# Kernel optimization log

Hardware: AMD Instinct MI355X
Metric: run time of the kernel (lower is better)

Reference implementation:

```python
import jax, jax.numpy as jnp
import numpy as np

IN_C = 32
OUT_C = 32
N_POLY = 3   # radial polynomial order
L_POLY = 3   # theta polynomial order
M_POLY = 3   # phi polynomial order
CONV_NUMS = 16
EPS = 1e-8


def _knn_select(pos, space_points_num, outpoint_num, conv_num):
    """Strided center sampling + KNN within each space. pos: [P,3].
    Returns global neighbor indices [space_num*outpoint_num, conv_num]."""
    P = pos.shape[0]
    S = P // space_points_num
    pos3 = pos.reshape(S, space_points_num, 3)
    stride = space_points_num // outpoint_num
    c_idx = jnp.arange(outpoint_num) * stride                       # [O]
    cpos = pos3[:, c_idx]                                           # [S,O,3]
    d2 = jnp.sum((cpos[:, :, None, :] - pos3[:, None, :, :]) ** 2, -1)  # [S,O,Ps]
    _, idx = jax.lax.top_k(-d2, conv_num)                           # [S,O,conv]
    idx = idx + (jnp.arange(S) * space_points_num)[:, None, None]
    return idx.reshape(S * outpoint_num, conv_num)


def _dcconv_forward(position_matrix, channel_matrix, coeff, bias, neighbor_indices, conv_num):
    K = neighbor_indices.shape[0]
    # --- CoordinateTransformer: gather, center, PCA rotate, spherical ---
    nbr = position_matrix[neighbor_indices]            # [K,conv,3]
    centers = nbr.mean(axis=1)                         # [K,3]
    local = nbr - centers[:, None, :]                  # [K,conv,3]
    cov = jnp.einsum('kci,kcj->kij', local, local) / conv_num
    _, V = jnp.linalg.eigh(cov)                        # [K,3,3] principal axes
    local_pca = jnp.einsum('kci,kij->kcj', local, V)   # rotate into PCA frame
    x, y, z = local_pca[..., 0], local_pca[..., 1], local_pca[..., 2]
    r = jnp.sqrt(x * x + y * y + z * z + EPS)          # [K,conv]
    theta = jnp.arccos(jnp.clip(z / r, -1.0, 1.0))
    phi = jnp.arctan2(y, x)
    # --- local features: [C_in, K, conv] (matches permute(2,0,1)) ---
    feat = channel_matrix[neighbor_indices].transpose(2, 0, 1)
    # --- DCConv3dKernelPolynomials: separable polynomial basis ---
    rp = r[..., None] ** jnp.arange(N_POLY, dtype=r.dtype)          # [K,conv,N]
    tp = theta[..., None] ** jnp.arange(L_POLY, dtype=r.dtype)      # [K,conv,L]
    pp = phi[..., None] ** jnp.arange(M_POLY, dtype=r.dtype)        # [K,conv,M]
    basis = jnp.einsum('kcn,kcl,kcm->kcnlm', rp, tp, pp)            # [K,conv,N,L,M]
    kernel_weights = jnp.einsum('kcnlm,oinlm->oikc', basis, coeff)  # [O,I,K,conv]
    # --- AggregationLayer: weighted sum over in-channels and neighbors ---
    out = jnp.einsum('ikc,oikc->ok', feat, kernel_weights)          # [O,K]
    output = out.T + bias                                           # [K,O]
    # --- resnet branch: all-ones kernel -> per-point feature sum ---
    resnet_output = jnp.broadcast_to(feat.sum(axis=(0, 2))[:, None], (K, OUT_C))
    return centers, output, resnet_output


def setup_inputs() -> dict:
    key = jax.random.key(0)
    k1, k2, k3 = jax.random.split(key, 3)
    P = 16384
    return {
        "position_matrix": jax.random.normal(k1, (P, 3), jnp.float32),
        "channel_matrix": jax.random.normal(k2, (P, IN_C), jnp.float32),
        "space_points_num": 1024,
        "outpoint_num": 256,
        "coeff": jax.random.normal(k3, (OUT_C, IN_C, N_POLY, L_POLY, M_POLY), jnp.float32) * 0.1,
        "bias": jnp.zeros((OUT_C,), jnp.float32),
    }


def reference(position_matrix, channel_matrix, space_points_num, outpoint_num, coeff, bias):
    conv_num = min(space_points_num - outpoint_num + 1, CONV_NUMS)
    neighbor_indices = _knn_select(position_matrix, space_points_num, outpoint_num, conv_num)
    return _dcconv_forward(position_matrix, channel_matrix, coeff, bias, neighbor_indices, conv_num)
```

## Files before the change

### kernel.cpp

```cpp
#include <hip/hip_runtime.h>
#include <math.h>

#define NSPACE 16
#define SPN    1024
#define OPN    256
#define STRIDE 4
#define CONV   16
#define KTOT   4096
#define INC    32
#define OUTC   32
#define NB     27
#define EPS_R  1e-8f

#define OFF_OUT 12288
#define OFF_RES 143360

typedef float v2f __attribute__((ext_vector_type(2)));

#define UPDPP __builtin_amdgcn_update_dpp

__device__ __forceinline__ float wave_min64_bcast(float m) {
  int t;
  t = UPDPP(__float_as_int(m), __float_as_int(m), 0x111, 0xf, 0xf, false);
  m = fminf(m, __int_as_float(t));
  t = UPDPP(__float_as_int(m), __float_as_int(m), 0x112, 0xf, 0xf, false);
  m = fminf(m, __int_as_float(t));
  t = UPDPP(__float_as_int(m), __float_as_int(m), 0x114, 0xf, 0xf, false);
  m = fminf(m, __int_as_float(t));
  t = UPDPP(__float_as_int(m), __float_as_int(m), 0x118, 0xf, 0xf, false);
  m = fminf(m, __int_as_float(t));
  t = UPDPP(__float_as_int(m), __float_as_int(m), 0x142, 0xa, 0xf, false);
  m = fminf(m, __int_as_float(t));
  t = UPDPP(__float_as_int(m), __float_as_int(m), 0x143, 0xc, 0xf, false);
  m = fminf(m, __int_as_float(t));
  return __int_as_float(__builtin_amdgcn_readlane(__float_as_int(m), 63));
}

__device__ __forceinline__ float wave_sum64_bcast(float m) {
  int t;
  t = UPDPP(0, __float_as_int(m), 0x111, 0xf, 0xf, true); m += __int_as_float(t);
  t = UPDPP(0, __float_as_int(m), 0x112, 0xf, 0xf, true); m += __int_as_float(t);
  t = UPDPP(0, __float_as_int(m), 0x114, 0xf, 0xf, true); m += __int_as_float(t);
  t = UPDPP(0, __float_as_int(m), 0x118, 0xf, 0xf, true); m += __int_as_float(t);
  t = UPDPP(0, __float_as_int(m), 0x142, 0xa, 0xf, true); m += __int_as_float(t);
  t = UPDPP(0, __float_as_int(m), 0x143, 0xc, 0xf, true); m += __int_as_float(t);
  return __int_as_float(__builtin_amdgcn_readlane(__float_as_int(m), 63));
}

__device__ __forceinline__ float group32_sum(float m) {
  int t;
  t = UPDPP(0, __float_as_int(m), 0x111, 0xf, 0xf, true); m += __int_as_float(t);
  t = UPDPP(0, __float_as_int(m), 0x112, 0xf, 0xf, true); m += __int_as_float(t);
  t = UPDPP(0, __float_as_int(m), 0x114, 0xf, 0xf, true); m += __int_as_float(t);
  t = UPDPP(0, __float_as_int(m), 0x118, 0xf, 0xf, true); m += __int_as_float(t);
  t = UPDPP(0, __float_as_int(m), 0x142, 0xa, 0xf, true); m += __int_as_float(t);
  return m;
}


#define EIGH_Z_PARAMS                                                         \
  float &z00, float &z01, float &z02, float &z10, float &z11, float &z12,     \
  float &z20, float &z21, float &z22
#define EIGH_Z_ARGS z00, z01, z02, z10, z11, z12, z20, z21, z22

#define ROT01(c, s)                                              \
  { float _t;                                                    \
    _t = z01; z01 = (c) * _t - (s) * z00; z00 = (s) * _t + (c) * z00; \
    _t = z11; z11 = (c) * _t - (s) * z10; z10 = (s) * _t + (c) * z10; \
    _t = z21; z21 = (c) * _t - (s) * z20; z20 = (s) * _t + (c) * z20; }
#define ROT12(c, s)                                              \
  { float _t;                                                    \
    _t = z02; z02 = (c) * _t - (s) * z01; z01 = (s) * _t + (c) * z01; \
    _t = z12; z12 = (c) * _t - (s) * z11; z11 = (s) * _t + (c) * z11; \
    _t = z22; z22 = (c) * _t - (s) * z21; z21 = (s) * _t + (c) * z21; }
#define SWAP01 { float _t; _t = z00; z00 = z01; z01 = _t; _t = z10; z10 = z11; z11 = _t; _t = z20; z20 = z21; z21 = _t; }
#define SWAP02 { float _t; _t = z00; z00 = z02; z02 = _t; _t = z10; z10 = z12; z12 = _t; _t = z20; z20 = z22; z22 = _t; }
#define SWAP12 { float _t; _t = z01; z01 = z02; z02 = _t; _t = z11; z11 = z12; z12 = _t; _t = z21; z21 = z22; z22 = _t; }

__device__ __forceinline__ float f_sign(float a, float b) {
  return (b >= 0.0f) ? fabsf(a) : -fabsf(a);
}

__device__ __forceinline__ float slapy2(float x, float y) {
  float xa = fabsf(x), ya = fabsf(y);
  float w = fmaxf(xa, ya), zz = fminf(xa, ya);
  if (zz == 0.0f) return w;
  float q = zz / w;
  return w * __fsqrt_rn(1.0f + q * q);
}

__device__ __forceinline__ void slartg_(float f, float g, float* c, float* s, float* r) {
  const float safmin = 1.1754943508e-38f;
  const float safmax = 8.5070591730e+37f;
  const float rtmin  = 1.0842021725e-19f;
  const float rtmax  = 9.2233720369e+18f;
  float f1 = fabsf(f), g1 = fabsf(g);
  if (g == 0.0f) {
    *c = 1.0f; *s = 0.0f; *r = f;
  } else if (f == 0.0f) {
    *c = 0.0f; *s = (g >= 0.0f) ? 1.0f : -1.0f; *r = g1;
  } else if (f1 > rtmin && f1 < rtmax && g1 > rtmin && g1 < rtmax) {
    float d = __fsqrt_rn(f * f + g * g);
    *c = f1 / d;
    *r = (f >= 0.0f) ? d : -d;
    *s = g / (*r);
  } else {
    float u = fminf(safmax, fmaxf(safmin, fmaxf(f1, g1)));
    float fs = f / u, gs = g / u;
    float d = __fsqrt_rn(fs * fs + gs * gs);
    *c = fabsf(fs) / d;
    float rr = (f >= 0.0f) ? d : -d;
    *s = gs / rr;
    *r = rr * u;
  }
}

__device__ __forceinline__ void slaev2_(float a, float b, float c,
                                        float* rt1, float* rt2, float* cs1, float* sn1) {
  float sm = a + c;
  float df = a - c;
  float adf = fabsf(df);
  float tb = b + b;
  float ab = fabsf(tb);
  float acmx, acmn;
  if (fabsf(a) > fabsf(c)) { acmx = a; acmn = c; } else { acmx = c; acmn = a; }
  float rt;
  if (adf > ab)      { float q = ab / adf; rt = adf * __fsqrt_rn(1.0f + q * q); }
  else if (adf < ab) { float q = adf / ab; rt = ab  * __fsqrt_rn(1.0f + q * q); }
  else               { rt = ab * __fsqrt_rn(2.0f); }
  int sgn1;
  if (sm < 0.0f) {
    *rt1 = 0.5f * (sm - rt); sgn1 = -1;
    *rt2 = (acmx / *rt1) * acmn - (b / *rt1) * b;
  } else if (sm > 0.0f) {
    *rt1 = 0.5f * (sm + rt); sgn1 = 1;
    *rt2 = (acmx / *rt1) * acmn - (b / *rt1) * b;
  } else {
    *rt1 = 0.5f * rt; *rt2 = -0.5f * rt; sgn1 = 1;
  }
  float cs; int sgn2;
  if (df >= 0.0f) { cs = df + rt; sgn2 = 1; } else { cs = df - rt; sgn2 = -1; }
  float acs = fabsf(cs);
  if (acs > ab) {
    float ct = -tb / cs;
    *sn1 = 1.0f / __fsqrt_rn(1.0f + ct * ct);
    *cs1 = ct * (*sn1);
  } else {
    if (ab == 0.0f) { *cs1 = 1.0f; *sn1 = 0.0f; }
    else {
      float tn = -cs / tb;
      *cs1 = 1.0f / __fsqrt_rn(1.0f + tn * tn);
      *sn1 = tn * (*cs1);
    }
  }
  if (sgn1 == sgn2) { float tn = *cs1; *cs1 = -(*sn1); *sn1 = tn; }
}

__device__ __forceinline__ void steqr2_01(float& dA, float& eA, float& dB,
                                          bool ql, EIGH_Z_PARAMS) {
  const float eps2 = 3.5527136788e-15f, safmin = 1.1754943508e-38f;
  float tst = eA * eA;
  float thr = ql ? (eps2 * fabsf(dA)) * fabsf(dB) + safmin
                 : (eps2 * fabsf(dB)) * fabsf(dA) + safmin;
  if (tst <= thr) { eA = 0.0f; return; }
  float rt1, rt2, c, s;
  slaev2_(dA, eA, dB, &rt1, &rt2, &c, &s);
  ROT01(c, s);
  dA = rt1; dB = rt2; eA = 0.0f;
}

__device__ __forceinline__ void steqr2_12(float& dA, float& eA, float& dB,
                                          bool ql, EIGH_Z_PARAMS) {
  const float eps2 = 3.5527136788e-15f, safmin = 1.1754943508e-38f;
  float tst = eA * eA;
  float thr = ql ? (eps2 * fabsf(dA)) * fabsf(dB) + safmin
                 : (eps2 * fabsf(dB)) * fabsf(dA) + safmin;
  if (tst <= thr) { eA = 0.0f; return; }
  float rt1, rt2, c, s;
  slaev2_(dA, eA, dB, &rt1, &rt2, &c, &s);
  ROT12(c, s);
  dA = rt1; dB = rt2; eA = 0.0f;
}

__device__ __forceinline__ void steqr_ql3(float& d1, float& d2, float& d3,
                                          float& e1, float& e2, int& jtot,
                                          EIGH_Z_PARAMS) {
  const float eps2 = 3.5527136788e-15f, safmin = 1.1754943508e-38f;
  int l = 1;
  while (true) {
    if (l == 1) {
      if (e1 * e1 <= (eps2 * fabsf(d1)) * fabsf(d2) + safmin) { e1 = 0.0f; l = 2; continue; }
      if (e2 * e2 <= (eps2 * fabsf(d2)) * fabsf(d3) + safmin) {
        e2 = 0.0f;
        float rt1, rt2, c, s;
        slaev2_(d1, e1, d2, &rt1, &rt2, &c, &s);
        ROT01(c, s);
        d1 = rt1; d2 = rt2; e1 = 0.0f;
        l = 3; continue;
      }
      if (jtot == 90) return;
      jtot++;
      float p = d1;
      float g = (d2 - p) / (2.0f * e1);
      float r = slapy2(g, 1.0f);
      g = d3 - p + (e1 / (g + f_sign(r, g)));
      float s = 1.0f, c = 1.0f; p = 0.0f;
      float f, b, wc1, wc2, ws1, ws2;
      f = s * e2; b = c * e2;
      slartg_(g, f, &c, &s, &r);
      g = d3 - p;
      r = (d2 - g) * s + 2.0f * c * b;
      p = s * r;
      d3 = g + p;
      g = c * r - b;
      wc2 = c; ws2 = -s;
      f = s * e1; b = c * e1;
      slartg_(g, f, &c, &s, &r);
      e2 = r;
      g = d2 - p;
      r = (d1 - g) * s + 2.0f * c * b;
      p = s * r;
      d2 = g + p;
      g = c * r - b;
      wc1 = c; ws1 = -s;
      if (wc2 != 1.0f || ws2 != 0.0f) ROT12(wc2, ws2);
      if (wc1 != 1.0f || ws1 != 0.0f) ROT01(wc1, ws1);
      d1 = d1 - p;
      e1 = g;
      continue;
    }
    if (l == 2) {
      if (e2 * e2 <= (eps2 * fabsf(d2)) * fabsf(d3) + safmin) { e2 = 0.0f; l = 3; continue; }
      float rt1, rt2, c, s;
      slaev2_(d2, e2, d3, &rt1, &rt2, &c, &s);
      ROT12(c, s);
      d2 = rt1; d3 = rt2; e2 = 0.0f;
      return;
    }
    return;
  }
}

__device__ __forceinline__ void steqr_qr3(float& d1, float& d2, float& d3,
                                          float& e1, float& e2, int& jtot,
                                          EIGH_Z_PARAMS) {
  const float eps2 = 3.5527136788e-15f, safmin = 1.1754943508e-38f;
  int l = 3;
  while (true) {
    if (l == 3) {
      if (e2 * e2 <= (eps2 * fabsf(d3)) * fabsf(d2) + safmin) { e2 = 0.0f; l = 2; continue; }
      if (e1 * e1 <= (eps2 * fabsf(d2)) * fabsf(d1) + safmin) {
        e1 = 0.0f;
        float rt1, rt2, c, s;
        slaev2_(d2, e2, d3, &rt1, &rt2, &c, &s);
        ROT12(c, s);
        d2 = rt1; d3 = rt2; e2 = 0.0f;
        l = 1; continue;
      }
      if (jtot == 90) return;
      jtot++;
      float p = d3;
      float g = (d2 - p) / (2.0f * e2);
      float r = slapy2(g, 1.0f);
      g = d1 - p + (e2 / (g + f_sign(r, g)));
      float s = 1.0f, c = 1.0f; p = 0.0f;
      float f, b, wc1, wc2, ws1, ws2;
      f = s * e1; b = c * e1;
      slartg_(g, f, &c, &s, &r);
      g = d1 - p;
      r = (d2 - g) * s + 2.0f * c * b;
      p = s * r;
      d1 = g + p;
      g = c * r - b;
      wc1 = c; ws1 = s;
      f = s * e2; b = c * e2;
      slartg_(g, f, &c, &s, &r);
      e1 = r;
      g = d2 - p;
      r = (d3 - g) * s + 2.0f * c * b;
      p = s * r;
      d2 = g + p;
      g = c * r - b;
      wc2 = c; ws2 = s;
      if (wc1 != 1.0f || ws1 != 0.0f) ROT01(wc1, ws1);
      if (wc2 != 1.0f || ws2 != 0.0f) ROT12(wc2, ws2);
      d3 = d3 - p;
      e2 = g;
      continue;
    }
    if (l == 2) {
      if (e1 * e1 <= (eps2 * fabsf(d2)) * fabsf(d1) + safmin) { e1 = 0.0f; l = 1; continue; }
      float rt1, rt2, c, s;
      slaev2_(d1, e1, d2, &rt1, &rt2, &c, &s);
      ROT01(c, s);
      d1 = rt1; d2 = rt2; e1 = 0.0f;
      return;
    }
    return;
  }
}

__device__ __forceinline__ void ssteqr3s(float& d1, float& d2, float& d3,
                                         float& e1, float& e2, EIGH_Z_PARAMS) {
  const float eps    = 5.9604644775e-08f;
  const float ssfmax = 3.0744573457e+18f;
  const float ssfmin = 3.0517578125e-05f;
  int jtot = 0;
  int m;
  {
    float tst = fabsf(e1);
    if (tst == 0.0f) m = 1;
    else if (tst <= (__fsqrt_rn(fabsf(d1)) * __fsqrt_rn(fabsf(d2))) * eps) { e1 = 0.0f; m = 1; }
    else {
      tst = fabsf(e2);
      if (tst == 0.0f) m = 2;
      else if (tst <= (__fsqrt_rn(fabsf(d2)) * __fsqrt_rn(fabsf(d3))) * eps) { e2 = 0.0f; m = 2; }
      else m = 3;
    }
  }
  if (m == 3) {
    float anorm = fmaxf(fmaxf(fabsf(d1), fabsf(d2)), fabsf(d3));
    anorm = fmaxf(anorm, fmaxf(fabsf(e1), fabsf(e2)));
    if (anorm != 0.0f) {
      int iscale = 0; float mul;
      if (anorm > ssfmax) {
        iscale = 1; mul = ssfmax / anorm;
        d1 *= mul; d2 *= mul; d3 *= mul; e1 *= mul; e2 *= mul;
      } else if (anorm < ssfmin) {
        iscale = 2; mul = ssfmin / anorm;
        d1 *= mul; d2 *= mul; d3 *= mul; e1 *= mul; e2 *= mul;
      }
      if (fabsf(d3) < fabsf(d1)) steqr_qr3(d1, d2, d3, e1, e2, jtot, EIGH_Z_ARGS);
      else                       steqr_ql3(d1, d2, d3, e1, e2, jtot, EIGH_Z_ARGS);
      if (iscale == 1) {
        mul = anorm / ssfmax;
        d1 *= mul; d2 *= mul; d3 *= mul; e1 *= mul; e2 *= mul;
      } else if (iscale == 2) {
        mul = anorm / ssfmin;
        d1 *= mul; d2 *= mul; d3 *= mul; e1 *= mul; e2 *= mul;
      }
    }
  } else if (m == 2) {
    float anorm = fmaxf(fmaxf(fabsf(d1), fabsf(d2)), fabsf(e1));
    if (anorm != 0.0f) {
      int iscale = 0; float mul;
      if (anorm > ssfmax) { iscale = 1; mul = ssfmax / anorm; d1 *= mul; d2 *= mul; e1 *= mul; }
      else if (anorm < ssfmin) { iscale = 2; mul = ssfmin / anorm; d1 *= mul; d2 *= mul; e1 *= mul; }
      steqr2_01(d1, e1, d2, !(fabsf(d2) < fabsf(d1)), EIGH_Z_ARGS);
      if (iscale == 1) { mul = anorm / ssfmax; d1 *= mul; d2 *= mul; e1 *= mul; }
      else if (iscale == 2) { mul = anorm / ssfmin; d1 *= mul; d2 *= mul; e1 *= mul; }
    }
  } else {
    int m2;
    float tst = fabsf(e2);
    if (tst == 0.0f) m2 = 2;
    else if (tst <= (__fsqrt_rn(fabsf(d2)) * __fsqrt_rn(fabsf(d3))) * eps) { e2 = 0.0f; m2 = 2; }
    else m2 = 3;
    if (m2 == 3) {
      float anorm = fmaxf(fmaxf(fabsf(d2), fabsf(d3)), fabsf(e2));
      if (anorm != 0.0f) {
        int iscale = 0; float mul;
        if (anorm > ssfmax) { iscale = 1; mul = ssfmax / anorm; d2 *= mul; d3 *= mul; e2 *= mul; }
        else if (anorm < ssfmin) { iscale = 2; mul = ssfmin / anorm; d2 *= mul; d3 *= mul; e2 *= mul; }
        steqr2_12(d2, e2, d3, !(fabsf(d3) < fabsf(d2)), EIGH_Z_ARGS);
        if (iscale == 1) { mul = anorm / ssfmax; d2 *= mul; d3 *= mul; e2 *= mul; }
        else if (iscale == 2) { mul = anorm / ssfmin; d2 *= mul; d3 *= mul; e2 *= mul; }
      }
    }
  }
  {
    int k = 1; float p = d1;
    if (d2 < p) { k = 2; p = d2; }
    if (d3 < p) { k = 3; p = d3; }
    if (k == 2)      { d2 = d1; d1 = p; SWAP01; }
    else if (k == 3) { d3 = d1; d1 = p; SWAP02; }
    if (d3 < d2) { p = d3; d3 = d2; d2 = p; SWAP12; }
  }
}

__device__ __forceinline__ void eigh3(float a11, float a21, float a31,
                                      float a22, float a32, float a33,
                                      EIGH_Z_PARAMS) {
  float tau1 = 0.0f, v3 = 0.0f, e1;
  float xnorm = fabsf(a31);
  if (xnorm == 0.0f) {
    tau1 = 0.0f;
    e1 = a21;
    v3 = 0.0f;
  } else {
    float beta = -f_sign(slapy2(a21, xnorm), a21);
    tau1 = (beta - a21) / beta;
    v3 = a31 / (a21 - beta);
    e1 = beta;
  }
  if (tau1 != 0.0f) {
    float x1 = tau1 * (a22 + a32 * v3);
    float x2 = tau1 * (a32 + a33 * v3);
    float alpha = -0.5f * tau1 * (x1 + x2 * v3);
    float w1 = x1 + alpha;
    float w2 = x2 + alpha * v3;
    a22 = a22 - w1 - w1;
    a32 = a32 - v3 * w1 - w2;
    a33 = a33 - v3 * w2 - w2 * v3;
  }
  float d1 = a11, d2 = a22, d3 = a33, e2 = a32;
  z00 = 1.0f; z01 = 0.0f; z02 = 0.0f;
  z10 = 0.0f; z11 = 1.0f; z12 = 0.0f;
  z20 = 0.0f; z21 = 0.0f; z22 = 1.0f;
  ssteqr3s(d1, d2, d3, e1, e2, EIGH_Z_ARGS);
  if (tau1 != 0.0f) {
    float tt;
    tt = z10 + v3 * z20; z10 -= tau1 * tt; z20 -= tau1 * tt * v3;
    tt = z11 + v3 * z21; z11 -= tau1 * tt; z21 -= tau1 * tt * v3;
    tt = z12 + v3 * z22; z12 -= tau1 * tt; z22 -= tau1 * tt * v3;
  }
}


#define CE(i, j)                                                  \
  {                                                               \
    unsigned long long ta = K[i], tb = K[j];                      \
    bool sw = tb < ta;                                            \
    K[i] = sw ? tb : ta;                                          \
    K[j] = sw ? ta : tb;                                          \
  }

#define RFL(x) __int_as_float(__builtin_amdgcn_readfirstlane(__float_as_int(x)))

__global__ __launch_bounds__(256, 4) void dcconv_fused(
    const float* __restrict__ pos, const float* __restrict__ chan,
    const float* __restrict__ coeff, const float* __restrict__ bias,
    float* __restrict__ out) {
  const int t    = threadIdx.x;
  const int wv   = t >> 6;
  const int lane = t & 63;
  const int kglob = blockIdx.x * 4 + wv;
  const int sp   = kglob >> 8;
  const int ci   = kglob & 255;
  const int base = sp * SPN;

  __shared__ __align__(16) float basis_sh[4][CONV][28];
  __shared__ __align__(16) float feat_sh[4][CONV][INC];
  __shared__ __align__(16) float G_sh[4][INC][28];

  const int cgl = base + ci * STRIDE;
  const float cx = pos[cgl * 3 + 0];
  const float cy = pos[cgl * 3 + 1];
  const float cz = pos[cgl * 3 + 2];

  unsigned long long K[16];
#pragma unroll
  for (int u = 0; u < 16; ++u) {
    const int j = u * 64 + lane;
    const float px = pos[(base + j) * 3 + 0];
    const float py = pos[(base + j) * 3 + 1];
    const float pz = pos[(base + j) * 3 + 2];
    float dx = __fsub_rn(cx, px), dy = __fsub_rn(cy, py), dz = __fsub_rn(cz, pz);
    float d2 = __fadd_rn(__fadd_rn(__fmul_rn(dx, dx), __fmul_rn(dy, dy)),
                         __fmul_rn(dz, dz));
    K[u] = (((unsigned long long)__float_as_uint(d2)) << 32) | (unsigned)j;
  }

  CE(0, 1) CE(2, 3) CE(4, 5) CE(6, 7) CE(8, 9) CE(10, 11) CE(12, 13) CE(14, 15)
  CE(0, 2) CE(1, 3) CE(4, 6) CE(5, 7) CE(8, 10) CE(9, 11) CE(12, 14) CE(13, 15)
  CE(1, 2) CE(5, 6) CE(9, 10) CE(13, 14)
  CE(0, 4) CE(1, 5) CE(2, 6) CE(3, 7) CE(8, 12) CE(9, 13) CE(10, 14) CE(11, 15)
  CE(2, 4) CE(3, 5) CE(10, 12) CE(11, 13)
  CE(1, 2) CE(3, 4) CE(5, 6) CE(9, 10) CE(11, 12) CE(13, 14)
  CE(0, 8) CE(1, 9) CE(2, 10) CE(3, 11) CE(4, 12) CE(5, 13) CE(6, 14) CE(7, 15)
  CE(4, 8) CE(5, 9) CE(6, 10) CE(7, 11)
  CE(2, 4) CE(3, 5) CE(6, 8) CE(7, 9) CE(10, 12) CE(11, 13)
  CE(1, 2) CE(3, 4) CE(5, 6) CE(7, 8) CE(9, 10) CE(11, 12) CE(13, 14)

  int myidx = cgl;
#pragma unroll 1
  for (int it = 0; it < CONV; ++it) {
    const float f0 = __uint_as_float((unsigned)(K[0] >> 32));
    const float m = wave_min64_bcast(f0);
    const unsigned long long msk = __ballot(f0 == m);
    const int wl = (int)__builtin_ctzll(msk);
    const int widx = __builtin_amdgcn_readlane((int)(unsigned)(K[0] & 0xffffffffu), wl);
    if (lane == it) myidx = base + widx;
    const bool on = (lane == wl);
#pragma unroll
    for (int u = 0; u < 15; ++u) K[u] = on ? K[u + 1] : K[u];
    K[15] = on ? ~0ull : K[15];
  }

  float nx = 0.0f, ny = 0.0f, nz = 0.0f;
  if (lane < CONV) {
    const float* pp = pos + myidx * 3;
    nx = pp[0]; ny = pp[1]; nz = pp[2];
  }

  const int hc = lane >> 5;
  const int ifeat = lane & 31;
  float fv0, fv1, fv2, fv3, fv4, fv5, fv6, fv7;
  {
    int g;
    g = __shfl(myidx,  0 + hc); fv0 = chan[g * INC + ifeat];
    g = __shfl(myidx,  2 + hc); fv1 = chan[g * INC + ifeat];
    g = __shfl(myidx,  4 + hc); fv2 = chan[g * INC + ifeat];
    g = __shfl(myidx,  6 + hc); fv3 = chan[g * INC + ifeat];
    g = __shfl(myidx,  8 + hc); fv4 = chan[g * INC + ifeat];
    g = __shfl(myidx, 10 + hc); fv5 = chan[g * INC + ifeat];
    g = __shfl(myidx, 12 + hc); fv6 = chan[g * INC + ifeat];
    g = __shfl(myidx, 14 + hc); fv7 = chan[g * INC + ifeat];
  }

  const float mx = wave_sum64_bcast(nx) * 0.0625f;
  const float my = wave_sum64_bcast(ny) * 0.0625f;
  const float mz = wave_sum64_bcast(nz) * 0.0625f;
  if (lane == 0) {
    out[kglob * 3 + 0] = mx; out[kglob * 3 + 1] = my; out[kglob * 3 + 2] = mz;
  }
  const float lx = nx - mx, ly = ny - my, lz = nz - mz;
  const float lxm = (lane < CONV) ? lx : 0.0f;
  const float lym = (lane < CONV) ? ly : 0.0f;
  const float lzm = (lane < CONV) ? lz : 0.0f;
  const float inv = 1.0f / (float)CONV;
  const float c00 = wave_sum64_bcast(lxm * lxm) * inv;
  const float c10 = wave_sum64_bcast(lym * lxm) * inv;
  const float c20 = wave_sum64_bcast(lzm * lxm) * inv;
  const float c11 = wave_sum64_bcast(lym * lym) * inv;
  const float c21 = wave_sum64_bcast(lzm * lym) * inv;
  const float c22 = wave_sum64_bcast(lzm * lzm) * inv;

  float V00 = 0, V01 = 0, V02 = 0, V10 = 0, V11 = 0, V12 = 0,
        V20 = 0, V21 = 0, V22 = 0;
  if (lane == 0) {
    eigh3(c00, c10, c20, c11, c21, c22,
          V00, V01, V02, V10, V11, V12, V20, V21, V22);
  }
  V00 = RFL(V00); V01 = RFL(V01); V02 = RFL(V02);
  V10 = RFL(V10); V11 = RFL(V11); V12 = RFL(V12);
  V20 = RFL(V20); V21 = RFL(V21); V22 = RFL(V22);

  if (lane < CONV) {
    float x = lx * V00 + ly * V10 + lz * V20;
    float y = lx * V01 + ly * V11 + lz * V21;
    float z = lx * V02 + ly * V12 + lz * V22;
    float r = __fsqrt_rn(x * x + y * y + z * z + EPS_R);
    float ct = fminf(fmaxf(z / r, -1.0f), 1.0f);
    float theta = acosf(ct);
    float phi = atan2f(y, x);
    const float r1 = r, r2 = r * r;
    const float t1 = theta, t2 = theta * theta;
    const float p1 = phi, p2 = phi * phi;
    float4* bp = (float4*)(&basis_sh[wv][lane][0]);
    bp[0] = make_float4(1.0f,      p1,        p2,        t1);
    bp[1] = make_float4(t1 * p1,   t1 * p2,   t2,        t2 * p1);
    bp[2] = make_float4(t2 * p2,   r1,        r1 * p1,   r1 * p2);
    bp[3] = make_float4(r1 * t1,   r1 * t1 * p1, r1 * t1 * p2, r1 * t2);
    bp[4] = make_float4(r1 * t2 * p1, r1 * t2 * p2, r2,  r2 * p1);
    bp[5] = make_float4(r2 * p2,   r2 * t1,   r2 * t1 * p1, r2 * t1 * p2);
    bp[6] = make_float4(r2 * t2,   r2 * t2 * p1, r2 * t2 * p2, 0.0f);
  }

  feat_sh[wv][ 0 + hc][ifeat] = fv0;
  feat_sh[wv][ 2 + hc][ifeat] = fv1;
  feat_sh[wv][ 4 + hc][ifeat] = fv2;
  feat_sh[wv][ 6 + hc][ifeat] = fv3;
  feat_sh[wv][ 8 + hc][ifeat] = fv4;
  feat_sh[wv][10 + hc][ifeat] = fv5;
  feat_sh[wv][12 + hc][ifeat] = fv6;
  feat_sh[wv][14 + hc][ifeat] = fv7;
  float s_loc = ((fv0 + fv1) + (fv2 + fv3)) + ((fv4 + fv5) + (fv6 + fv7));
  const float sres = wave_sum64_bcast(s_loc);
  if (lane < OUTC) out[OFF_RES + kglob * OUTC + lane] = sres;

  {
    const int gi = lane >> 1;
    const int jh = lane & 1;
    const int jr0 = jh ? 12 : 0;
    v2f a2[8];
#pragma unroll
    for (int q = 0; q < 8; ++q) a2[q] = (v2f)(0.0f);
#pragma unroll
    for (int c = 0; c < CONV; ++c) {
      const float f = feat_sh[wv][c][gi];
      const v2f f2 = (v2f)(f);
      const float4* bp = (const float4*)(&basis_sh[wv][c][jr0]);
#pragma unroll
      for (int q = 0; q < 4; ++q) {
        const float4 v4 = bp[q];
        v2f blo; blo.x = v4.x; blo.y = v4.y;
        v2f bhi; bhi.x = v4.z; bhi.y = v4.w;
        a2[2 * q + 0] += f2 * blo;
        a2[2 * q + 1] += f2 * bhi;
      }
    }
    if (jh == 0) {
      float4* gp = (float4*)(&G_sh[wv][gi][0]);
      gp[0] = make_float4(a2[0].x, a2[0].y, a2[1].x, a2[1].y);
      gp[1] = make_float4(a2[2].x, a2[2].y, a2[3].x, a2[3].y);
      gp[2] = make_float4(a2[4].x, a2[4].y, a2[5].x, a2[5].y);
      gp[3] = make_float4(a2[6].x, a2[6].y, a2[7].x, a2[7].y);
    } else {
      float4* gp = (float4*)(&G_sh[wv][gi][16]);
      gp[0] = make_float4(a2[2].x, a2[2].y, a2[3].x, a2[3].y);
      gp[1] = make_float4(a2[4].x, a2[4].y, a2[5].x, a2[5].y);
      gp[2] = make_float4(a2[6].x, a2[6].y, a2[7].x, a2[7].y);
    }
  }

  __syncthreads();

  {
    const int ir = t & 31;
    const int oh = t >> 5;
    const int l32 = lane & 31;
#pragma unroll
    for (int p = 0; p < 2; ++p) {
      const int o0 = oh * 4 + p * 2;
      const float* cA = coeff + (o0 * INC + ir) * NB;
      const float* cB = coeff + ((o0 + 1) * INC + ir) * NB;
      v2f c0p[14], c1p[14];
#pragma unroll
      for (int q = 0; q < 13; ++q) {
        c0p[q].x = cA[2 * q]; c0p[q].y = cA[2 * q + 1];
        c1p[q].x = cB[2 * q]; c1p[q].y = cB[2 * q + 1];
      }
      c0p[13].x = cA[26]; c0p[13].y = 0.0f;
      c1p[13].x = cB[26]; c1p[13].y = 0.0f;
      float s0c0 = 0, s0c1 = 0, s0c2 = 0, s0c3 = 0;
      float s1c0 = 0, s1c1 = 0, s1c2 = 0, s1c3 = 0;
#pragma unroll
      for (int cc = 0; cc < 4; ++cc) {
        const float4* gp = (const float4*)(&G_sh[cc][ir][0]);
        v2f a0 = (v2f)(0.0f), a1 = (v2f)(0.0f);
#pragma unroll
        for (int q = 0; q < 7; ++q) {
          const float4 v4 = gp[q];
          v2f glo; glo.x = v4.x; glo.y = v4.y;
          v2f ghi; ghi.x = v4.z; ghi.y = v4.w;
          a0 += glo * c0p[2 * q + 0];
          a0 += ghi * c0p[2 * q + 1];
          a1 += glo * c1p[2 * q + 0];
          a1 += ghi * c1p[2 * q + 1];
        }
        const float s0 = a0.x + a0.y;
        const float s1 = a1.x + a1.y;
        if (cc == 0) { s0c0 = s0; s1c0 = s1; }
        else if (cc == 1) { s0c1 = s0; s1c1 = s1; }
        else if (cc == 2) { s0c2 = s0; s1c2 = s1; }
        else { s0c3 = s0; s1c3 = s1; }
      }
      s0c0 = group32_sum(s0c0); s0c1 = group32_sum(s0c1);
      s0c2 = group32_sum(s0c2); s0c3 = group32_sum(s0c3);
      s1c0 = group32_sum(s1c0); s1c1 = group32_sum(s1c1);
      s1c2 = group32_sum(s1c2); s1c3 = group32_sum(s1c3);
      if (l32 == 31) {
        const float b0 = bias[o0], b1 = bias[o0 + 1];
        const int kb = blockIdx.x * 4;
        out[OFF_OUT + (kb + 0) * OUTC + o0] = s0c0 + b0;
        out[OFF_OUT + (kb + 1) * OUTC + o0] = s0c1 + b0;
        out[OFF_OUT + (kb + 2) * OUTC + o0] = s0c2 + b0;
        out[OFF_OUT + (kb + 3) * OUTC + o0] = s0c3 + b0;
        out[OFF_OUT + (kb + 0) * OUTC + o0 + 1] = s1c0 + b1;
        out[OFF_OUT + (kb + 1) * OUTC + o0 + 1] = s1c1 + b1;
        out[OFF_OUT + (kb + 2) * OUTC + o0 + 1] = s1c2 + b1;
        out[OFF_OUT + (kb + 3) * OUTC + o0 + 1] = s1c3 + b1;
      }
    }
  }
}

extern "C" void kernel_launch(void* const* d_in, const int* in_sizes, int n_in,
                              void* d_out, int out_size, void* d_ws, size_t ws_size,
                              hipStream_t stream) {
  const float* pos   = (const float*)d_in[0];
  const float* chan  = (const float*)d_in[1];
  const float* coeff = (const float*)d_in[4];
  const float* bias  = (const float*)d_in[5];
  float* out = (float*)d_out;
  dcconv_fused<<<dim3(KTOT / 4), dim3(256), 0, stream>>>(pos, chan, coeff, bias, out);
}
```

Baseline: 34.26 us.

## Flatten G to contiguous IN*NB layout and contract coeff rows with float4 loads

The per-channel G matrix is stored densely as a flat [INC*27] array per wave instead of padded rows of 28. The final contraction is remapped so each group of 8 threads owns one output channel and streams that channel's 864 coefficients as coalesced float4 loads. This replaces strided scalar coefficient loads and 32-lane reductions with a reduction over 8 lanes. In exchange, G is now written with scalar LDS stores and the float4 LDS reads of G may hit more bank conflicts.

```diff
diff --git a/kernel.cpp b/kernel.cpp
--- a/kernel.cpp
+++ b/kernel.cpp
@@ -47,13 +47,11 @@
   return __int_as_float(__builtin_amdgcn_readlane(__float_as_int(m), 63));
 }
 
-__device__ __forceinline__ float group32_sum(float m) {
+__device__ __forceinline__ float group8_sum(float m) {
   int t;
   t = UPDPP(0, __float_as_int(m), 0x111, 0xf, 0xf, true); m += __int_as_float(t);
   t = UPDPP(0, __float_as_int(m), 0x112, 0xf, 0xf, true); m += __int_as_float(t);
   t = UPDPP(0, __float_as_int(m), 0x114, 0xf, 0xf, true); m += __int_as_float(t);
-  t = UPDPP(0, __float_as_int(m), 0x118, 0xf, 0xf, true); m += __int_as_float(t);
-  t = UPDPP(0, __float_as_int(m), 0x142, 0xa, 0xf, true); m += __int_as_float(t);
   return m;
 }
 
@@ -441,7 +439,7 @@
 
   __shared__ __align__(16) float basis_sh[4][CONV][28];
   __shared__ __align__(16) float feat_sh[4][CONV][INC];
-  __shared__ __align__(16) float G_sh[4][INC][28];
+  __shared__ __align__(16) float G4_sh[4][INC * NB];
 
   const int cgl = base + ci * STRIDE;
   const float cx = pos[cgl * 3 + 0];
@@ -590,78 +588,64 @@
         a2[2 * q + 1] += f2 * bhi;
       }
     }
+    float* gq = &G4_sh[wv][gi * NB];
     if (jh == 0) {
-      float4* gp = (float4*)(&G_sh[wv][gi][0]);
-      gp[0] = make_float4(a2[0].x, a2[0].y, a2[1].x, a2[1].y);
-      gp[1] = make_float4(a2[2].x, a2[2].y, a2[3].x, a2[3].y);
-      gp[2] = make_float4(a2[4].x, a2[4].y, a2[5].x, a2[5].y);
-      gp[3] = make_float4(a2[6].x, a2[6].y, a2[7].x, a2[7].y);
+#pragma unroll
+      for (int jj = 0; jj < 14; ++jj)
+        gq[jj] = (jj & 1) ? a2[jj >> 1].y : a2[jj >> 1].x;
     } else {
-      float4* gp = (float4*)(&G_sh[wv][gi][16]);
-      gp[0] = make_float4(a2[2].x, a2[2].y, a2[3].x, a2[3].y);
-      gp[1] = make_float4(a2[4].x, a2[4].y, a2[5].x, a2[5].y);
-      gp[2] = make_float4(a2[6].x, a2[6].y, a2[7].x, a2[7].y);
+#pragma unroll
+      for (int jj = 14; jj < 27; ++jj) {
+        const int m = jj - 12;
+        gq[jj] = (m & 1) ? a2[m >> 1].y : a2[m >> 1].x;
+      }
     }
   }
 
   __syncthreads();
 
   {
-    const int ir = t & 31;
-    const int oh = t >> 5;
-    const int l32 = lane & 31;
-#pragma unroll
-    for (int p = 0; p < 2; ++p) {
-      const int o0 = oh * 4 + p * 2;
-      const float* cA = coeff + (o0 * INC + ir) * NB;
-      const float* cB = coeff + ((o0 + 1) * INC + ir) * NB;
-      v2f c0p[14], c1p[14];
-#pragma unroll
-      for (int q = 0; q < 13; ++q) {
-        c0p[q].x = cA[2 * q]; c0p[q].y = cA[2 * q + 1];
-        c1p[q].x = cB[2 * q]; c1p[q].y = cB[2 * q + 1];
-      }
-      c0p[13].x = cA[26]; c0p[13].y = 0.0f;
-      c1p[13].x = cB[26]; c1p[13].y = 0.0f;
-      float s0c0 = 0, s0c1 = 0, s0c2 = 0, s0c3 = 0;
-      float s1c0 = 0, s1c1 = 0, s1c2 = 0, s1c3 = 0;
-#pragma unroll
-      for (int cc = 0; cc < 4; ++cc) {
-        const float4* gp = (const float4*)(&G_sh[cc][ir][0]);
-        v2f a0 = (v2f)(0.0f), a1 = (v2f)(0.0f);
-#pragma unroll
-        for (int q = 0; q < 7; ++q) {
-          const float4 v4 = gp[q];
-          v2f glo; glo.x = v4.x; glo.y = v4.y;
-          v2f ghi; ghi.x = v4.z; ghi.y = v4.w;
-          a0 += glo * c0p[2 * q + 0];
-          a0 += ghi * c0p[2 * q + 1];
-          a1 += glo * c1p[2 * q + 0];
-          a1 += ghi * c1p[2 * q + 1];
-        }
-        const float s0 = a0.x + a0.y;
-        const float s1 = a1.x + a1.y;
-        if (cc == 0) { s0c0 = s0; s1c0 = s1; }
-        else if (cc == 1) { s0c1 = s0; s1c1 = s1; }
-        else if (cc == 2) { s0c2 = s0; s1c2 = s1; }
-        else { s0c3 = s0; s1c3 = s1; }
-      }
-      s0c0 = group32_sum(s0c0); s0c1 = group32_sum(s0c1);
-      s0c2 = group32_sum(s0c2); s0c3 = group32_sum(s0c3);
-      s1c0 = group32_sum(s1c0); s1c1 = group32_sum(s1c1);
-      s1c2 = group32_sum(s1c2); s1c3 = group32_sum(s1c3);
-      if (l32 == 31) {
-        const float b0 = bias[o0], b1 = bias[o0 + 1];
-        const int kb = blockIdx.x * 4;
-        out[OFF_OUT + (kb + 0) * OUTC + o0] = s0c0 + b0;
-        out[OFF_OUT + (kb + 1) * OUTC + o0] = s0c1 + b0;
-        out[OFF_OUT + (kb + 2) * OUTC + o0] = s0c2 + b0;
-        out[OFF_OUT + (kb + 3) * OUTC + o0] = s0c3 + b0;
-        out[OFF_OUT + (kb + 0) * OUTC + o0 + 1] = s1c0 + b1;
-        out[OFF_OUT + (kb + 1) * OUTC + o0 + 1] = s1c1 + b1;
-        out[OFF_OUT + (kb + 2) * OUTC + o0 + 1] = s1c2 + b1;
-        out[OFF_OUT + (kb + 3) * OUTC + o0 + 1] = s1c3 + b1;
-      }
+    const int o = t >> 3;
+    const int q = t & 7;
+    const float4* arow = (const float4*)(coeff + o * (INC * NB));
+    const float4* g0 = (const float4*)(&G4_sh[0][0]);
+    const float4* g1 = (const float4*)(&G4_sh[1][0]);
+    const float4* g2 = (const float4*)(&G4_sh[2][0]);
+    const float4* g3 = (const float4*)(&G4_sh[3][0]);
+    v2f ac0 = (v2f)(0.0f), ac1 = (v2f)(0.0f), ac2 = (v2f)(0.0f), ac3 = (v2f)(0.0f);
+#pragma unroll 3
+    for (int k = 0; k < 27; ++k) {
+      const int f4 = k * 8 + q;
+      const float4 A = arow[f4];
+      v2f Alo; Alo.x = A.x; Alo.y = A.y;
+      v2f Ahi; Ahi.x = A.z; Ahi.y = A.w;
+      float4 Gv; v2f Glo, Ghi;
+      Gv = g0[f4];
+      Glo.x = Gv.x; Glo.y = Gv.y; Ghi.x = Gv.z; Ghi.y = Gv.w;
+      ac0 += Alo * Glo; ac0 += Ahi * Ghi;
+      Gv = g1[f4];
+      Glo.x = Gv.x; Glo.y = Gv.y; Ghi.x = Gv.z; Ghi.y = Gv.w;
+      ac1 += Alo * Glo; ac1 += Ahi * Ghi;
+      Gv = g2[f4];
+      Glo.x = Gv.x; Glo.y = Gv.y; Ghi.x = Gv.z; Ghi.y = Gv.w;
+      ac2 += Alo * Glo; ac2 += Ahi * Ghi;
+      Gv = g3[f4];
+      Glo.x = Gv.x; Glo.y = Gv.y; Ghi.x = Gv.z; Ghi.y = Gv.w;
+      ac3 += Alo * Glo; ac3 += Ahi * Ghi;
+    }
+    float s0 = ac0.x + ac0.y;
+    float s1 = ac1.x + ac1.y;
+    float s2 = ac2.x + ac2.y;
+    float s3 = ac3.x + ac3.y;
+    s0 = group8_sum(s0); s1 = group8_sum(s1);
+    s2 = group8_sum(s2); s3 = group8_sum(s3);
+    if (q == 7) {
+      const float b = bias[o];
+      const int kb = blockIdx.x * 4;
+      out[OFF_OUT + (kb + 0) * OUTC + o] = s0 + b;
+      out[OFF_OUT + (kb + 1) * OUTC + o] = s1 + b;
+      out[OFF_OUT + (kb + 2) * OUTC + o] = s2 + b;
+      out[OFF_OUT + (kb + 3) * OUTC + o] = s3 + b;
     }
   }
 }
```

Result: faster. 33.53 us (median of 2 runs) (-2.1%).
